# Optimization experiments

Measured on AMD Instinct MI355X. Metric: run time of the kernel, lower is better.

## Reference

```python
import jax, jax.numpy as jnp
import numpy as np

B, M, N = 4, 1024, 4096
DQ, DC, H, DH = 512, 512, 8, 64
D = H * DH
NEG = -10000000.0


def setup_inputs() -> dict:
    key = jax.random.key(0)
    ks = jax.random.split(key, 7)
    left = jax.random.normal(ks[0], (B, M, DQ), dtype=jnp.float32)
    right = jax.random.normal(ks[1], (B, N, DC), dtype=jnp.float32)
    mask = jax.random.randint(ks[2], (B, M, N), 0, 2).astype(bool)
    # learned params (torch Linear stores weight as (out,in); we store (in,out))
    Wq = jax.random.normal(ks[3], (DQ, D), dtype=jnp.float32) * (DQ ** -0.5)
    Wkv = jax.random.normal(ks[4], (DC, 2 * D), dtype=jnp.float32) * (DC ** -0.5)
    Wout = jax.random.normal(ks[5], (D, DQ), dtype=jnp.float32) * (D ** -0.5)
    bout = jax.random.normal(ks[6], (DQ,), dtype=jnp.float32) * 0.01
    return {"left": left, "right": right, "mask": mask,
            "Wq": Wq, "Wkv": Wkv, "Wout": Wout, "bout": bout}


def reference(left, right, mask, Wq, Wkv, Wout, bout):
    scale = DH ** -0.5
    q = left @ Wq                      # (B, M, D)
    kv = right @ Wkv                   # (B, N, 2D)
    k, v = jnp.split(kv, 2, axis=-1)   # (B, N, D) each
    q = q.reshape(B, M, H, DH).transpose(0, 2, 1, 3)  # (B, H, M, DH)
    k = k.reshape(B, N, H, DH).transpose(0, 2, 1, 3)  # (B, H, N, DH)
    v = v.reshape(B, N, H, DH).transpose(0, 2, 1, 3)  # (B, H, N, DH)
    sim = scale * jnp.einsum('bhmd,bhnd->bhmn', q, k)  # (B, H, M, N)
    sim = jnp.where(mask[:, None, :, :], sim, NEG)
    attn = jax.nn.softmax(sim, axis=-1)
    out = jnp.einsum('bhmn,bhnd->bhmd', attn, v)       # (B, H, M, DH)
    out = out.transpose(0, 2, 1, 3).reshape(B, M, D)
    return out @ Wout + bout           # (B, M, DQ)
```

## Files before the change

kernel.cpp:

```cpp
#include <hip/hip_runtime.h>

typedef _Float16 f16;
typedef __attribute__((ext_vector_type(8))) _Float16 half8;
typedef __attribute__((ext_vector_type(4))) _Float16 half4;
typedef __attribute__((ext_vector_type(4))) float floatx4;
typedef unsigned int uint32;
typedef __attribute__((ext_vector_type(4))) uint32 uint4v;

#define MFMA16(a, b, c) __builtin_amdgcn_mfma_f32_16x16x32_f16((a), (b), (c), 0, 0, 0)

constexpr int B_ = 4, M_ = 1024, N_ = 4096, DQ_ = 512, DC_ = 512, H_ = 8, DH_ = 64, D_ = 512;
constexpr int KP_ = 576;
constexpr int VP_ = 4224;
constexpr int NSPLIT = 4;
constexpr float QSC_ = 0.18033688011112042f;

typedef __attribute__((address_space(1))) const void glds_g;
typedef __attribute__((address_space(3))) void glds_l;
__device__ __forceinline__ void g2lds16(const void* g, void* l) {
    __builtin_amdgcn_global_load_lds((glds_g*)g, (glds_l*)l, 16, 0, 0);
}

__device__ __forceinline__ void wtr_tile(const float* __restrict__ src, f16* __restrict__ dst,
                                         int Nout, int bx, int by, int tid) {
    __shared__ __align__(16) f16 Ts[64][72];
    const int n0 = bx * 64, k0 = by * 64;
    {
        int kr = tid >> 2, q4 = tid & 3;
        const float* sp = src + (size_t)(k0 + kr) * Nout + n0 + q4 * 16;
        float4 x0 = *(const float4*)(sp + 0), x1 = *(const float4*)(sp + 4);
        float4 x2 = *(const float4*)(sp + 8), x3 = *(const float4*)(sp + 12);
        half8 h0, h1;
        h0[0]=(f16)x0.x; h0[1]=(f16)x0.y; h0[2]=(f16)x0.z; h0[3]=(f16)x0.w;
        h0[4]=(f16)x1.x; h0[5]=(f16)x1.y; h0[6]=(f16)x1.z; h0[7]=(f16)x1.w;
        h1[0]=(f16)x2.x; h1[1]=(f16)x2.y; h1[2]=(f16)x2.z; h1[3]=(f16)x2.w;
        h1[4]=(f16)x3.x; h1[5]=(f16)x3.y; h1[6]=(f16)x3.z; h1[7]=(f16)x3.w;
        *(half8*)&Ts[kr][q4 * 16] = h0;
        *(half8*)&Ts[kr][q4 * 16 + 8] = h1;
    }
    __syncthreads();
    {
        int nr = tid >> 2, q = tid & 3;
        half8 h0, h1;
#pragma unroll
        for (int j = 0; j < 8; j++) { h0[j] = Ts[q * 16 + j][nr]; h1[j] = Ts[q * 16 + 8 + j][nr]; }
        f16* dp = dst + (size_t)(n0 + nr) * 512 + k0 + q * 16;
        *(half8*)(dp + 0) = h0;
        *(half8*)(dp + 8) = h1;
    }
}

__global__ __launch_bounds__(256)
void prep_k(const void* __restrict__ mask, uint32* __restrict__ bits,
            const float* __restrict__ left, f16* __restrict__ leftb,
            const float* __restrict__ right, f16* __restrict__ rightb,
            const float* __restrict__ Wq, f16* __restrict__ wqt,
            const float* __restrict__ Wkv, f16* __restrict__ wkvt,
            const float* __restrict__ Wout, f16* __restrict__ woutt) {
    const int blk = blockIdx.x, tid = threadIdx.x;
    if (blk < 4096) {
        __shared__ int s_bad;
        if (tid == 0) s_bad = 0;
        __syncthreads();
        const uint32* w = (const uint32*)mask + (size_t)blk * 1024;
        int bad = 0;
#pragma unroll
        for (int j = 0; j < 4; j++) bad |= (w[tid * 4 + j] & 0xFFFFFFFEu) != 0u;
        if (bad) s_bad = 1;
        __syncthreads();
        const bool bytes_mode = s_bad != 0;
        const size_t base = (size_t)blk * 4096;
        const int lane = tid & 63;
        for (int j = 0; j < 16; j++) {
            size_t e = base + j * 256 + tid;
            bool pred = bytes_mode ? (((const unsigned char*)mask)[e] != 0)
                                   : (((const int*)mask)[e] != 0);
            unsigned long long bal = __ballot(pred);
            if (lane == 0)       bits[e >> 5] = (uint32)bal;
            else if (lane == 32) bits[e >> 5] = (uint32)(bal >> 32);
        }
    } else if (blk < 6144) {
        int i = ((blk - 4096) * 256 + tid) * 4;
        float4 x = *(const float4*)(left + i);
        half4 h; h[0] = (f16)x.x; h[1] = (f16)x.y; h[2] = (f16)x.z; h[3] = (f16)x.w;
        *(half4*)(leftb + i) = h;
    } else if (blk < 14336) {
        int i = ((blk - 6144) * 256 + tid) * 4;
        float4 x = *(const float4*)(right + i);
        half4 h; h[0] = (f16)x.x; h[1] = (f16)x.y; h[2] = (f16)x.z; h[3] = (f16)x.w;
        *(half4*)(rightb + i) = h;
    } else if (blk < 14400) {
        int r = blk - 14336;
        wtr_tile(Wq, wqt, 512, r & 7, r >> 3, tid);
    } else if (blk < 14528) {
        int r = blk - 14400;
        wtr_tile(Wkv, wkvt, 1024, r & 15, r >> 4, tid);
    } else {
        int r = blk - 14528;
        wtr_tile(Wout, woutt, 512, r & 7, r >> 3, tid);
    }
}

__global__ __launch_bounds__(256)
void gemmqkv_k(const f16* __restrict__ leftb, const f16* __restrict__ wqt,
               const f16* __restrict__ rightb, const f16* __restrict__ wkvt,
               f16* __restrict__ qb, f16* __restrict__ kb, f16* __restrict__ vt) {
    __shared__ __align__(16) f16 As[128 * 64];
    __shared__ __align__(16) f16 Bs[128 * 64];
    const int blk = blockIdx.x, tid = threadIdx.x;
    const int lane = tid & 63, wave = tid >> 6;
    const int qd = lane >> 4, l16 = lane & 15;
    const int wm = wave >> 1, wn = wave & 1;

    int mode;
    const f16* A; const f16* Bt; size_t m0, n0;
    if (blk < 1024) {
        size_t rows = (size_t)(blk & 127) * 128, cols = (size_t)(blk >> 7) * 128;
        if (cols < 512) { mode = 0; A = rightb; m0 = rows; Bt = wkvt;   n0 = cols; }
        else            { mode = 1; A = wkvt;   m0 = cols; Bt = rightb; n0 = rows; }
    } else {
        int r = blk - 1024;
        mode = 2; A = leftb; Bt = wqt;
        m0 = (size_t)(r & 31) * 128; n0 = (size_t)(r >> 5) * 128;
    }

    size_t goff[4];
    f16 *la[4], *lb[4];
#pragma unroll
    for (int i = 0; i < 4; i++) {
        int c = i * 256 + wave * 64 + lane;
        int row = c >> 3, col8 = (c & 7) ^ (row & 7);
        goff[i] = (size_t)row * 512 + col8 * 8;
        la[i] = As + (size_t)(i * 256 + wave * 64) * 8;
        lb[i] = Bs + (size_t)(i * 256 + wave * 64) * 8;
    }
    const f16* Ab = A + m0 * 512;
    const f16* Bb = Bt + n0 * 512;

    floatx4 acc[4][4] = {};

    for (int k0 = 0; k0 < 512; k0 += 64) {
        __syncthreads();
#pragma unroll
        for (int i = 0; i < 4; i++) g2lds16(Ab + goff[i] + k0, la[i]);
#pragma unroll
        for (int i = 0; i < 4; i++) g2lds16(Bb + goff[i] + k0, lb[i]);
        __syncthreads();
#pragma unroll
        for (int kk = 0; kk < 2; kk++) {
            half8 a[4], b[4];
#pragma unroll
            for (int t = 0; t < 4; t++) {
                int rowa = wm * 64 + t * 16 + l16;
                int rowb = wn * 64 + t * 16 + l16;
                int pa8 = ((kk * 4 + qd) ^ (rowa & 7)) * 8;
                int pb8 = ((kk * 4 + qd) ^ (rowb & 7)) * 8;
                a[t] = *(const half8*)&As[rowa * 64 + pa8];
                b[t] = *(const half8*)&Bs[rowb * 64 + pb8];
            }
#pragma unroll
            for (int mt = 0; mt < 4; mt++)
#pragma unroll
                for (int nt = 0; nt < 4; nt++)
                    acc[mt][nt] = MFMA16(a[mt], b[nt], acc[mt][nt]);
        }
    }

#pragma unroll
    for (int mt = 0; mt < 4; mt++)
#pragma unroll
        for (int nt = 0; nt < 4; nt++)
#pragma unroll
            for (int r = 0; r < 4; r++) {
                size_t mi = m0 + wm * 64 + mt * 16 + qd * 4 + r;
                size_t ni = n0 + wn * 64 + nt * 16 + l16;
                float v = acc[mt][nt][r];
                if (mode == 2) {
                    qb[mi * 512 + ni] = (f16)v;
                } else if (mode == 0) {
                    kb[mi * KP_ + ni] = (f16)v;
                } else {
                    int dcol = (int)mi - 512;
                    int hh = dcol >> 6, dh = dcol & 63;
                    size_t bb = ni >> 12, nn = ni & 4095;
                    vt[((bb * H_ + hh) * (size_t)DH_ + dh) * VP_ + nn] = (f16)v;
                }
            }
}

__global__ __launch_bounds__(256)
void attn_k(const f16* __restrict__ Qb, const f16* __restrict__ Kb,
            const f16* __restrict__ Vt, const uint32* __restrict__ mb,
            float* __restrict__ Op, float* __restrict__ Lp) {
    const int tid = threadIdx.x;
    const int lane = tid & 63, wave = tid >> 6;
    const int qd = lane >> 4, l16 = lane & 15;
    const int bh = blockIdx.x, b = bh >> 3, h = bh & 7;
    const int z = blockIdx.z;
    constexpr int iters = N_ / (64 * NSPLIT);
    const int n_base = z * iters * 64;
    const int m_base = blockIdx.y * 128 + wave * 32;

    __shared__ __align__(16) f16 Ks[2][64 * 64];
    __shared__ __align__(16) f16 Vs[2][64 * 64];

    half8 q[2][2];
#pragma unroll
    for (int f = 0; f < 2; f++) {
        const f16* qrow = Qb + ((size_t)(b * M_ + m_base + f * 16 + l16)) * D_ + h * DH_;
        half8 r0 = *(const half8*)(qrow + qd * 8);
        half8 r1 = *(const half8*)(qrow + 32 + qd * 8);
#pragma unroll
        for (int j = 0; j < 8; j++) {
            q[f][0][j] = (f16)((float)r0[j] * QSC_);
            q[f][1][j] = (f16)((float)r1[j] * QSC_);
        }
    }
    const half8 ONE = {(f16)1, (f16)1, (f16)1, (f16)1, (f16)1, (f16)1, (f16)1, (f16)1};

    floatx4 ot[2][4] = {};
    floatx4 ol[2] = {};

    const uint32* mrow0 = mb + ((size_t)(b * M_ + m_base + l16)) * (N_ / 32);
    const uint32* mrow1 = mrow0 + (size_t)16 * (N_ / 32);

    const int srow = wave * 16;
    const int r8 = lane >> 3, p8 = lane & 7;
    const int gc8 = p8 ^ r8;
    const f16* kg = Kb + ((size_t)(b * N_) + srow + r8) * KP_ + h * DH_ + gc8 * 8;
    const f16* vg = Vt + ((size_t)(bh * DH_) + srow + r8) * VP_ + gc8 * 8;

    auto stage = [&](int buf, int n0) {
#pragma unroll
        for (int j = 0; j < 2; j++) {
            g2lds16(kg + ((size_t)n0 + j * 8) * KP_, &Ks[buf][(srow + j * 8) * 64]);
            g2lds16(vg + (size_t)(j * 8) * VP_ + n0, &Vs[buf][(srow + j * 8) * 64]);
        }
    };

    stage(0, n_base);
    int cur = 0;

    for (int it = 0; it < iters; it++) {
        const int n0 = n_base + it * 64;
        uint2 mm0 = *(const uint2*)(mrow0 + (n0 >> 5));
        uint2 mm1 = *(const uint2*)(mrow1 + (n0 >> 5));
        __syncthreads();
        if (it + 1 < iters) stage(cur ^ 1, n0 + 64);

        uint32 u[2][2] = {{mm0.x >> (qd * 4), mm0.y >> (qd * 4)},
                          {mm1.x >> (qd * 4), mm1.y >> (qd * 4)}};

        uint32 pk[2][4][2];
#pragma unroll
        for (int s = 0; s < 4; s++) {
            const int ro = (s * 16 + l16) * 64;
            half8 k0 = *(const half8*)&Ks[cur][ro + (((qd) ^ (l16 & 7)) * 8)];
            half8 k1 = *(const half8*)&Ks[cur][ro + (((4 + qd) ^ (l16 & 7)) * 8)];
#pragma unroll
            for (int f = 0; f < 2; f++) {
                floatx4 t = {};
                t = MFMA16(k0, q[f][0], t);
                t = MFMA16(k1, q[f][1], t);
                uint32 us = u[f][s >> 1] >> ((s & 1) * 16);
                float e0 = __builtin_amdgcn_exp2f(t[0]);
                float e1 = __builtin_amdgcn_exp2f(t[1]);
                float e2 = __builtin_amdgcn_exp2f(t[2]);
                float e3 = __builtin_amdgcn_exp2f(t[3]);
                e0 = (us & 1u) ? e0 : 0.0f;
                e1 = (us & 2u) ? e1 : 0.0f;
                e2 = (us & 4u) ? e2 : 0.0f;
                e3 = (us & 8u) ? e3 : 0.0f;
                pk[f][s][0] = __builtin_bit_cast(uint32, __builtin_amdgcn_cvt_pkrtz(e0, e1));
                pk[f][s][1] = __builtin_bit_cast(uint32, __builtin_amdgcn_cvt_pkrtz(e2, e3));
            }
        }

        half8 pa[2][2];
#pragma unroll
        for (int f = 0; f < 2; f++) {
#pragma unroll
            for (int hh = 0; hh < 2; hh++) {
                uint32 w0, w1, w2, w3;
                {
                    auto a = __builtin_amdgcn_permlane32_swap(pk[f][2 * hh][0], pk[f][2 * hh + 1][0], false, false);
                    auto c = __builtin_amdgcn_permlane16_swap(a[0], a[1], false, false);
                    w0 = c[0]; w2 = c[1];
                }
                {
                    auto a = __builtin_amdgcn_permlane32_swap(pk[f][2 * hh][1], pk[f][2 * hh + 1][1], false, false);
                    auto c = __builtin_amdgcn_permlane16_swap(a[0], a[1], false, false);
                    w1 = c[0]; w3 = c[1];
                }
                uint4v wv = {w0, w1, w2, w3};
                pa[f][hh] = __builtin_bit_cast(half8, wv);
            }
        }

#pragma unroll
        for (int f = 0; f < 2; f++) {
            ol[f] = MFMA16(ONE, pa[f][0], ol[f]);
            ol[f] = MFMA16(ONE, pa[f][1], ol[f]);
        }
#pragma unroll
        for (int sd = 0; sd < 4; sd++) {
            const int ro = (sd * 16 + l16) * 64;
            half8 v0 = *(const half8*)&Vs[cur][ro + (((qd) ^ (l16 & 7)) * 8)];
            half8 v1 = *(const half8*)&Vs[cur][ro + (((4 + qd) ^ (l16 & 7)) * 8)];
#pragma unroll
            for (int f = 0; f < 2; f++) {
                ot[f][sd] = MFMA16(v0, pa[f][0], ot[f][sd]);
                ot[f][sd] = MFMA16(v1, pa[f][1], ot[f][sd]);
            }
        }
        cur ^= 1;
    }

#pragma unroll
    for (int f = 0; f < 2; f++) {
        size_t row = (size_t)(z * 32 + bh) * M_ + m_base + f * 16 + l16;
        float* op = Op + row * DH_ + qd * 4;
#pragma unroll
        for (int sd = 0; sd < 4; sd++)
            __builtin_nontemporal_store(ot[f][sd], (floatx4*)(op + sd * 16));
        if (qd == 0) __builtin_nontemporal_store(ol[f][0], Lp + row);
    }
}

__global__ __launch_bounds__(256)
void comb_k(const float* __restrict__ Op, const float* __restrict__ Lp, f16* __restrict__ Ob,
            int nsp) {
    int i = blockIdx.x * 256 + threadIdx.x;
    int d4 = i & 15, m = (i >> 4) & 1023, bh = i >> 14;
    float nx = 0.f, ny = 0.f, nz = 0.f, nw = 0.f, den = 0.f;
    for (int s = 0; s < nsp; s++) {
        size_t row = ((size_t)s * 32 + bh) * M_ + m;
        float4 x = *(const float4*)(Op + row * DH_ + d4 * 4);
        nx += x.x; ny += x.y; nz += x.z; nw += x.w;
        den += Lp[row];
    }
    float r = 1.0f / den;
    int b = bh >> 3, h = bh & 7;
    f16* o = Ob + ((size_t)(b * M_ + m)) * D_ + h * DH_ + d4 * 4;
    half4 hv; hv[0] = (f16)(nx * r); hv[1] = (f16)(ny * r); hv[2] = (f16)(nz * r); hv[3] = (f16)(nw * r);
    *(half4*)o = hv;
}

__global__ __launch_bounds__(256)
void gemmout_k(const f16* __restrict__ A, const f16* __restrict__ Bt,
               float* __restrict__ Fout, const float* __restrict__ bias) {
    __shared__ __align__(16) f16 As[128 * 32];
    __shared__ __align__(16) f16 Bs[128 * 32];
    const int tid = threadIdx.x;
    const int lane = tid & 63, wave = tid >> 6;
    const int qd = lane >> 4, l16 = lane & 15;
    const int wm = wave >> 1, wn = wave & 1;
    const size_t m0 = (size_t)blockIdx.x * 128;
    const size_t n0 = (size_t)blockIdx.y * 128;

    const int c1 = wave * 64 + lane;
    const int c2 = 256 + c1;
    f16* la1 = As + (size_t)(wave * 64) * 8;
    f16* la2 = As + (size_t)(256 + wave * 64) * 8;
    f16* lb1 = Bs + (size_t)(wave * 64) * 8;
    f16* lb2 = Bs + (size_t)(256 + wave * 64) * 8;

    floatx4 acc[4][4] = {};

    for (int k0 = 0; k0 < 512; k0 += 32) {
        __syncthreads();
        g2lds16(A + (m0 + (c1 >> 2)) * 512 + k0 + (c1 & 3) * 8, la1);
        g2lds16(A + (m0 + (c2 >> 2)) * 512 + k0 + (c2 & 3) * 8, la2);
        g2lds16(Bt + (n0 + (c1 >> 2)) * 512 + k0 + (c1 & 3) * 8, lb1);
        g2lds16(Bt + (n0 + (c2 >> 2)) * 512 + k0 + (c2 & 3) * 8, lb2);
        __syncthreads();
        half8 a[4], b[4];
#pragma unroll
        for (int t = 0; t < 4; t++) {
            a[t] = *(const half8*)&As[(wm * 64 + t * 16 + l16) * 32 + qd * 8];
            b[t] = *(const half8*)&Bs[(wn * 64 + t * 16 + l16) * 32 + qd * 8];
        }
#pragma unroll
        for (int mt = 0; mt < 4; mt++)
#pragma unroll
            for (int nt = 0; nt < 4; nt++)
                acc[mt][nt] = MFMA16(a[mt], b[nt], acc[mt][nt]);
    }

#pragma unroll
    for (int mt = 0; mt < 4; mt++)
#pragma unroll
        for (int nt = 0; nt < 4; nt++)
#pragma unroll
            for (int r = 0; r < 4; r++) {
                size_t row = m0 + wm * 64 + mt * 16 + qd * 4 + r;
                size_t col = n0 + wn * 64 + nt * 16 + l16;
                Fout[row * 512 + col] = acc[mt][nt][r] + bias[col];
            }
}

extern "C" void kernel_launch(void* const* d_in, const int* in_sizes, int n_in,
                              void* d_out, int out_size, void* d_ws, size_t ws_size,
                              hipStream_t stream) {
    const float* left  = (const float*)d_in[0];
    const float* right = (const float*)d_in[1];
    const void*  mask  = d_in[2];
    const float* Wq    = (const float*)d_in[3];
    const float* Wkv   = (const float*)d_in[4];
    const float* Wout  = (const float*)d_in[5];
    const float* bout  = (const float*)d_in[6];

    char* ws = (char*)d_ws;
    size_t off = 0;
    auto take = [&](size_t bytes) { char* p = ws + off; off += (bytes + 255) & ~(size_t)255; return p; };
    uint32* mbits = (uint32*)take((size_t)B_ * M_ * N_ / 8);
    f16* woutt = (f16*)take((size_t)D_ * DQ_ * 2);
    f16* qb    = (f16*)take((size_t)B_ * M_ * D_ * 2);
    f16* kb    = (f16*)take((size_t)B_ * N_ * KP_ * 2);
    f16* vt    = (f16*)take((size_t)B_ * H_ * DH_ * VP_ * 2);
    f16* ob    = (f16*)take((size_t)B_ * M_ * D_ * 2);
    char* pool = (char*)take((size_t)34 * 1024 * 1024);
    f16* leftb  = (f16*)pool;
    f16* rightb = (f16*)(pool + (size_t)4 * 1024 * 1024);
    f16* wqt    = (f16*)(pool + (size_t)20 * 1024 * 1024);
    f16* wkvt   = (f16*)(pool + (size_t)21 * 1024 * 1024);
    float* Op   = (float*)pool;
    float* Lp   = (float*)(pool + (size_t)NSPLIT * 32 * M_ * DH_ * 4);

    prep_k<<<14592, 256, 0, stream>>>(mask, mbits, left, leftb, right, rightb,
                                      Wq, wqt, Wkv, wkvt, Wout, woutt);
    gemmqkv_k<<<1152, 256, 0, stream>>>(leftb, wqt, rightb, wkvt, qb, kb, vt);
    attn_k<<<dim3(32, 8, NSPLIT), 256, 0, stream>>>(qb, kb, vt, mbits, Op, Lp);
    comb_k<<<2048, 256, 0, stream>>>(Op, Lp, ob, NSPLIT);
    gemmout_k<<<dim3(32, 4), 256, 0, stream>>>(ob, woutt, (float*)d_out, bout);
}
```

Measured before the change: 271.5 us.

## Use 8 waves per attention block with one row-tile each, retile output GEMM

The attention kernel moves to 512 threads per block, with each wave handling 16 query rows instead of 32. This shrinks per-thread register use and raises occupancy. The softmax denominator is now summed with scalar adds and cross-lane shuffles instead of a ones-matrix MFMA, and the next mask word is prefetched one iteration ahead. The output GEMM switches from 128x128x32 tiles to 64x64x64 tiles with XOR-swizzled LDS to get more blocks and fewer bank conflicts, at the cost of less K/V and operand reuse per wave.

```diff
diff --git a/kernel.cpp b/kernel.cpp
--- a/kernel.cpp
+++ b/kernel.cpp
@@ -188,7 +188,7 @@
             }
 }
 
-__global__ __launch_bounds__(256)
+__global__ __launch_bounds__(512, 8)
 void attn_k(const f16* __restrict__ Qb, const f16* __restrict__ Kb,
             const f16* __restrict__ Vt, const uint32* __restrict__ mb,
             float* __restrict__ Op, float* __restrict__ Lp) {
@@ -199,131 +199,120 @@
     const int z = blockIdx.z;
     constexpr int iters = N_ / (64 * NSPLIT);
     const int n_base = z * iters * 64;
-    const int m_base = blockIdx.y * 128 + wave * 32;
+    const int m_base = blockIdx.y * 128 + wave * 16;
 
     __shared__ __align__(16) f16 Ks[2][64 * 64];
     __shared__ __align__(16) f16 Vs[2][64 * 64];
 
-    half8 q[2][2];
-#pragma unroll
-    for (int f = 0; f < 2; f++) {
-        const f16* qrow = Qb + ((size_t)(b * M_ + m_base + f * 16 + l16)) * D_ + h * DH_;
+    half8 q0, q1;
+    {
+        const f16* qrow = Qb + ((size_t)(b * M_ + m_base + l16)) * D_ + h * DH_;
         half8 r0 = *(const half8*)(qrow + qd * 8);
         half8 r1 = *(const half8*)(qrow + 32 + qd * 8);
 #pragma unroll
         for (int j = 0; j < 8; j++) {
-            q[f][0][j] = (f16)((float)r0[j] * QSC_);
-            q[f][1][j] = (f16)((float)r1[j] * QSC_);
-        }
-    }
-    const half8 ONE = {(f16)1, (f16)1, (f16)1, (f16)1, (f16)1, (f16)1, (f16)1, (f16)1};
-
-    floatx4 ot[2][4] = {};
-    floatx4 ol[2] = {};
-
-    const uint32* mrow0 = mb + ((size_t)(b * M_ + m_base + l16)) * (N_ / 32);
-    const uint32* mrow1 = mrow0 + (size_t)16 * (N_ / 32);
-
-    const int srow = wave * 16;
+            q0[j] = (f16)((float)r0[j] * QSC_);
+            q1[j] = (f16)((float)r1[j] * QSC_);
+        }
+    }
+
+    floatx4 ot[4] = {};
+    float l_acc = 0.0f;
+
+    const uint32* mrow = mb + ((size_t)(b * M_ + m_base + l16)) * (N_ / 32);
+
+    const int srow = wave * 8;
     const int r8 = lane >> 3, p8 = lane & 7;
     const int gc8 = p8 ^ r8;
     const f16* kg = Kb + ((size_t)(b * N_) + srow + r8) * KP_ + h * DH_ + gc8 * 8;
     const f16* vg = Vt + ((size_t)(bh * DH_) + srow + r8) * VP_ + gc8 * 8;
 
     auto stage = [&](int buf, int n0) {
-#pragma unroll
-        for (int j = 0; j < 2; j++) {
-            g2lds16(kg + ((size_t)n0 + j * 8) * KP_, &Ks[buf][(srow + j * 8) * 64]);
-            g2lds16(vg + (size_t)(j * 8) * VP_ + n0, &Vs[buf][(srow + j * 8) * 64]);
-        }
+        g2lds16(kg + (size_t)n0 * KP_, &Ks[buf][srow * 64]);
+        g2lds16(vg + n0, &Vs[buf][srow * 64]);
     };
 
     stage(0, n_base);
+    uint2 mmc = *(const uint2*)(mrow + (n_base >> 5));
     int cur = 0;
+
+    const int swz = (l16 & 7);
 
     for (int it = 0; it < iters; it++) {
         const int n0 = n_base + it * 64;
-        uint2 mm0 = *(const uint2*)(mrow0 + (n0 >> 5));
-        uint2 mm1 = *(const uint2*)(mrow1 + (n0 >> 5));
-        __syncthreads();
-        if (it + 1 < iters) stage(cur ^ 1, n0 + 64);
-
-        uint32 u[2][2] = {{mm0.x >> (qd * 4), mm0.y >> (qd * 4)},
-                          {mm1.x >> (qd * 4), mm1.y >> (qd * 4)}};
-
-        uint32 pk[2][4][2];
+        __syncthreads();
+        uint2 mmn;
+        if (it + 1 < iters) {
+            stage(cur ^ 1, n0 + 64);
+            mmn = *(const uint2*)(mrow + ((n0 + 64) >> 5));
+        }
+
+        const uint32 u0 = mmc.x >> (qd * 4);
+        const uint32 u1 = mmc.y >> (qd * 4);
+
+        uint32 pk[4][2];
 #pragma unroll
         for (int s = 0; s < 4; s++) {
             const int ro = (s * 16 + l16) * 64;
-            half8 k0 = *(const half8*)&Ks[cur][ro + (((qd) ^ (l16 & 7)) * 8)];
-            half8 k1 = *(const half8*)&Ks[cur][ro + (((4 + qd) ^ (l16 & 7)) * 8)];
-#pragma unroll
-            for (int f = 0; f < 2; f++) {
-                floatx4 t = {};
-                t = MFMA16(k0, q[f][0], t);
-                t = MFMA16(k1, q[f][1], t);
-                uint32 us = u[f][s >> 1] >> ((s & 1) * 16);
-                float e0 = __builtin_amdgcn_exp2f(t[0]);
-                float e1 = __builtin_amdgcn_exp2f(t[1]);
-                float e2 = __builtin_amdgcn_exp2f(t[2]);
-                float e3 = __builtin_amdgcn_exp2f(t[3]);
-                e0 = (us & 1u) ? e0 : 0.0f;
-                e1 = (us & 2u) ? e1 : 0.0f;
-                e2 = (us & 4u) ? e2 : 0.0f;
-                e3 = (us & 8u) ? e3 : 0.0f;
-                pk[f][s][0] = __builtin_bit_cast(uint32, __builtin_amdgcn_cvt_pkrtz(e0, e1));
-                pk[f][s][1] = __builtin_bit_cast(uint32, __builtin_amdgcn_cvt_pkrtz(e2, e3));
-            }
-        }
-
-        half8 pa[2][2];
-#pragma unroll
-        for (int f = 0; f < 2; f++) {
-#pragma unroll
-            for (int hh = 0; hh < 2; hh++) {
-                uint32 w0, w1, w2, w3;
-                {
-                    auto a = __builtin_amdgcn_permlane32_swap(pk[f][2 * hh][0], pk[f][2 * hh + 1][0], false, false);
-                    auto c = __builtin_amdgcn_permlane16_swap(a[0], a[1], false, false);
-                    w0 = c[0]; w2 = c[1];
-                }
-                {
-                    auto a = __builtin_amdgcn_permlane32_swap(pk[f][2 * hh][1], pk[f][2 * hh + 1][1], false, false);
-                    auto c = __builtin_amdgcn_permlane16_swap(a[0], a[1], false, false);
-                    w1 = c[0]; w3 = c[1];
-                }
-                uint4v wv = {w0, w1, w2, w3};
-                pa[f][hh] = __builtin_bit_cast(half8, wv);
-            }
-        }
-
-#pragma unroll
-        for (int f = 0; f < 2; f++) {
-            ol[f] = MFMA16(ONE, pa[f][0], ol[f]);
-            ol[f] = MFMA16(ONE, pa[f][1], ol[f]);
-        }
+            half8 k0 = *(const half8*)&Ks[cur][ro + ((qd ^ swz) * 8)];
+            half8 k1 = *(const half8*)&Ks[cur][ro + (((4 + qd) ^ swz) * 8)];
+            floatx4 t = {};
+            t = MFMA16(k0, q0, t);
+            t = MFMA16(k1, q1, t);
+            uint32 us = (s & 2 ? u1 : u0) >> ((s & 1) * 16);
+            float e0 = __builtin_amdgcn_exp2f(t[0]);
+            float e1 = __builtin_amdgcn_exp2f(t[1]);
+            float e2 = __builtin_amdgcn_exp2f(t[2]);
+            float e3 = __builtin_amdgcn_exp2f(t[3]);
+            e0 = (us & 1u) ? e0 : 0.0f;
+            e1 = (us & 2u) ? e1 : 0.0f;
+            e2 = (us & 4u) ? e2 : 0.0f;
+            e3 = (us & 8u) ? e3 : 0.0f;
+            l_acc += (e0 + e1) + (e2 + e3);
+            pk[s][0] = __builtin_bit_cast(uint32, __builtin_amdgcn_cvt_pkrtz(e0, e1));
+            pk[s][1] = __builtin_bit_cast(uint32, __builtin_amdgcn_cvt_pkrtz(e2, e3));
+        }
+
+        half8 pa[2];
+#pragma unroll
+        for (int hh = 0; hh < 2; hh++) {
+            uint32 w0, w1, w2, w3;
+            {
+                auto a = __builtin_amdgcn_permlane32_swap(pk[2 * hh][0], pk[2 * hh + 1][0], false, false);
+                auto c = __builtin_amdgcn_permlane16_swap(a[0], a[1], false, false);
+                w0 = c[0]; w2 = c[1];
+            }
+            {
+                auto a = __builtin_amdgcn_permlane32_swap(pk[2 * hh][1], pk[2 * hh + 1][1], false, false);
+                auto c = __builtin_amdgcn_permlane16_swap(a[0], a[1], false, false);
+                w1 = c[0]; w3 = c[1];
+            }
+            uint4v wv = {w0, w1, w2, w3};
+            pa[hh] = __builtin_bit_cast(half8, wv);
+        }
+
 #pragma unroll
         for (int sd = 0; sd < 4; sd++) {
             const int ro = (sd * 16 + l16) * 64;
-            half8 v0 = *(const half8*)&Vs[cur][ro + (((qd) ^ (l16 & 7)) * 8)];
-            half8 v1 = *(const half8*)&Vs[cur][ro + (((4 + qd) ^ (l16 & 7)) * 8)];
-#pragma unroll
-            for (int f = 0; f < 2; f++) {
-                ot[f][sd] = MFMA16(v0, pa[f][0], ot[f][sd]);
-                ot[f][sd] = MFMA16(v1, pa[f][1], ot[f][sd]);
-            }
-        }
+            half8 v0 = *(const half8*)&Vs[cur][ro + ((qd ^ swz) * 8)];
+            half8 v1 = *(const half8*)&Vs[cur][ro + (((4 + qd) ^ swz) * 8)];
+            ot[sd] = MFMA16(v0, pa[0], ot[sd]);
+            ot[sd] = MFMA16(v1, pa[1], ot[sd]);
+        }
+        mmc = mmn;
         cur ^= 1;
     }
 
-#pragma unroll
-    for (int f = 0; f < 2; f++) {
-        size_t row = (size_t)(z * 32 + bh) * M_ + m_base + f * 16 + l16;
+    l_acc += __shfl_xor(l_acc, 16);
+    l_acc += __shfl_xor(l_acc, 32);
+
+    {
+        size_t row = (size_t)(z * 32 + bh) * M_ + m_base + l16;
         float* op = Op + row * DH_ + qd * 4;
 #pragma unroll
         for (int sd = 0; sd < 4; sd++)
-            __builtin_nontemporal_store(ot[f][sd], (floatx4*)(op + sd * 16));
-        if (qd == 0) __builtin_nontemporal_store(ol[f][0], Lp + row);
+            __builtin_nontemporal_store(ot[sd], (floatx4*)(op + sd * 16));
+        if (qd == 0) __builtin_nontemporal_store(l_acc, Lp + row);
     }
 }
 
@@ -349,52 +338,65 @@
 __global__ __launch_bounds__(256)
 void gemmout_k(const f16* __restrict__ A, const f16* __restrict__ Bt,
                float* __restrict__ Fout, const float* __restrict__ bias) {
-    __shared__ __align__(16) f16 As[128 * 32];
-    __shared__ __align__(16) f16 Bs[128 * 32];
+    __shared__ __align__(16) f16 As[64 * 64];
+    __shared__ __align__(16) f16 Bs[64 * 64];
     const int tid = threadIdx.x;
     const int lane = tid & 63, wave = tid >> 6;
     const int qd = lane >> 4, l16 = lane & 15;
     const int wm = wave >> 1, wn = wave & 1;
-    const size_t m0 = (size_t)blockIdx.x * 128;
-    const size_t n0 = (size_t)blockIdx.y * 128;
-
-    const int c1 = wave * 64 + lane;
-    const int c2 = 256 + c1;
-    f16* la1 = As + (size_t)(wave * 64) * 8;
-    f16* la2 = As + (size_t)(256 + wave * 64) * 8;
-    f16* lb1 = Bs + (size_t)(wave * 64) * 8;
-    f16* lb2 = Bs + (size_t)(256 + wave * 64) * 8;
-
-    floatx4 acc[4][4] = {};
-
-    for (int k0 = 0; k0 < 512; k0 += 32) {
-        __syncthreads();
-        g2lds16(A + (m0 + (c1 >> 2)) * 512 + k0 + (c1 & 3) * 8, la1);
-        g2lds16(A + (m0 + (c2 >> 2)) * 512 + k0 + (c2 & 3) * 8, la2);
-        g2lds16(Bt + (n0 + (c1 >> 2)) * 512 + k0 + (c1 & 3) * 8, lb1);
-        g2lds16(Bt + (n0 + (c2 >> 2)) * 512 + k0 + (c2 & 3) * 8, lb2);
-        __syncthreads();
-        half8 a[4], b[4];
-#pragma unroll
-        for (int t = 0; t < 4; t++) {
-            a[t] = *(const half8*)&As[(wm * 64 + t * 16 + l16) * 32 + qd * 8];
-            b[t] = *(const half8*)&Bs[(wn * 64 + t * 16 + l16) * 32 + qd * 8];
-        }
-#pragma unroll
-        for (int mt = 0; mt < 4; mt++)
-#pragma unroll
-            for (int nt = 0; nt < 4; nt++)
-                acc[mt][nt] = MFMA16(a[mt], b[nt], acc[mt][nt]);
-    }
-
-#pragma unroll
-    for (int mt = 0; mt < 4; mt++)
-#pragma unroll
-        for (int nt = 0; nt < 4; nt++)
+    const size_t m0 = (size_t)blockIdx.x * 64;
+    const size_t n0 = (size_t)blockIdx.y * 64;
+
+    size_t goff[2];
+    f16 *la[2], *lb[2];
+#pragma unroll
+    for (int i = 0; i < 2; i++) {
+        int c = i * 256 + wave * 64 + lane;
+        int row = c >> 3, col8 = (c & 7) ^ (row & 7);
+        goff[i] = (size_t)row * 512 + col8 * 8;
+        la[i] = As + (size_t)(i * 256 + wave * 64) * 8;
+        lb[i] = Bs + (size_t)(i * 256 + wave * 64) * 8;
+    }
+    const f16* Ab = A + m0 * 512;
+    const f16* Bb = Bt + n0 * 512;
+
+    floatx4 acc[2][2] = {};
+
+    for (int k0 = 0; k0 < 512; k0 += 64) {
+        __syncthreads();
+#pragma unroll
+        for (int i = 0; i < 2; i++) g2lds16(Ab + goff[i] + k0, la[i]);
+#pragma unroll
+        for (int i = 0; i < 2; i++) g2lds16(Bb + goff[i] + k0, lb[i]);
+        __syncthreads();
+#pragma unroll
+        for (int kk = 0; kk < 2; kk++) {
+            half8 a[2], b[2];
+#pragma unroll
+            for (int t = 0; t < 2; t++) {
+                int rowa = wm * 32 + t * 16 + l16;
+                int rowb = wn * 32 + t * 16 + l16;
+                int pa8 = ((kk * 4 + qd) ^ (rowa & 7)) * 8;
+                int pb8 = ((kk * 4 + qd) ^ (rowb & 7)) * 8;
+                a[t] = *(const half8*)&As[rowa * 64 + pa8];
+                b[t] = *(const half8*)&Bs[rowb * 64 + pb8];
+            }
+#pragma unroll
+            for (int mt = 0; mt < 2; mt++)
+#pragma unroll
+                for (int nt = 0; nt < 2; nt++)
+                    acc[mt][nt] = MFMA16(a[mt], b[nt], acc[mt][nt]);
+        }
+    }
+
+#pragma unroll
+    for (int mt = 0; mt < 2; mt++)
+#pragma unroll
+        for (int nt = 0; nt < 2; nt++)
 #pragma unroll
             for (int r = 0; r < 4; r++) {
-                size_t row = m0 + wm * 64 + mt * 16 + qd * 4 + r;
-                size_t col = n0 + wn * 64 + nt * 16 + l16;
+                size_t row = m0 + wm * 32 + mt * 16 + qd * 4 + r;
+                size_t col = n0 + wn * 32 + nt * 16 + l16;
                 Fout[row * 512 + col] = acc[mt][nt][r] + bias[col];
             }
 }
@@ -430,7 +432,7 @@
     prep_k<<<14592, 256, 0, stream>>>(mask, mbits, left, leftb, right, rightb,
                                       Wq, wqt, Wkv, wkvt, Wout, woutt);
     gemmqkv_k<<<1152, 256, 0, stream>>>(leftb, wqt, rightb, wkvt, qb, kb, vt);
-    attn_k<<<dim3(32, 8, NSPLIT), 256, 0, stream>>>(qb, kb, vt, mbits, Op, Lp);
+    attn_k<<<dim3(32, 8, NSPLIT), 512, 0, stream>>>(qb, kb, vt, mbits, Op, Lp);
     comb_k<<<2048, 256, 0, stream>>>(Op, Lp, ob, NSPLIT);
-    gemmout_k<<<dim3(32, 4), 256, 0, stream>>>(ob, woutt, (float*)d_out, bout);
-}
+    gemmout_k<<<dim3(64, 8), 256, 0, stream>>>(ob, woutt, (float*)d_out, bout);
+}
```

Measured after the change: 271.6 us. About the same (+0.0%).
